# Kernel tuning notes

Measured on AMD Instinct MI355X. Metric: run time of the kernel, lower is better.

## Reference

```python
import jax, jax.numpy as jnp
import numpy as np

BN_EPS = 1e-5

def _bn(x, gamma, beta):
    # BatchNorm1d in training mode: batch mean, biased variance
    m = jnp.mean(x, axis=0)
    v = jnp.var(x, axis=0)
    return (x - m) * jax.lax.rsqrt(v + BN_EPS) * gamma + beta

def setup_inputs() -> dict:
    key = jax.random.key(0)
    ks = jax.random.split(key, 12)
    N, E, D, ED = 50000, 600000, 128, 16
    s = lambda k, sh: jax.random.normal(k, sh, dtype=jnp.float32) * 0.05
    return {
        'h': jax.random.normal(ks[0], (N, D), dtype=jnp.float32),
        'edge_index': jax.random.randint(ks[1], (2, E), 0, N, dtype=jnp.int64),
        'edge_attr': jax.random.normal(ks[2], (E, ED), dtype=jnp.float32),
        'ee_w1': s(ks[3], (ED, D)), 'ee_b1': jnp.zeros((D,), jnp.float32),
        'ee_g1': jnp.ones((D,), jnp.float32), 'ee_bb1': jnp.zeros((D,), jnp.float32),
        'ee_w2': s(ks[4], (D, D)), 'ee_b2': jnp.zeros((D,), jnp.float32),
        'mlp_w1': s(ks[5], (D, D)), 'mlp_b1': jnp.zeros((D,), jnp.float32),
        'mlp_g1': jnp.ones((D,), jnp.float32), 'mlp_bb1': jnp.zeros((D,), jnp.float32),
        'mlp_w2': s(ks[6], (D, D)), 'mlp_b2': jnp.zeros((D,), jnp.float32),
        'mlp_g2': jnp.ones((D,), jnp.float32), 'mlp_bb2': jnp.zeros((D,), jnp.float32),
    }

def reference(h, edge_index, edge_attr, ee_w1, ee_b1, ee_g1, ee_bb1, ee_w2, ee_b2,
              mlp_w1, mlp_b1, mlp_g1, mlp_bb1, mlp_w2, mlp_b2, mlp_g2, mlp_bb2):
    N = h.shape[0]
    src, dst = edge_index[0], edge_index[1]
    # edge_encoder: Linear -> BN -> ReLU -> Linear
    e = jax.nn.relu(_bn(edge_attr @ ee_w1 + ee_b1, ee_g1, ee_bb1)) @ ee_w2 + ee_b2  # [E, D]
    # scatter-add edge embeddings to destination nodes
    agg_edge = jax.ops.segment_sum(e, dst, num_segments=N)  # [N, D]
    h = h + agg_edge
    # GINConv (eps=0): mlp(h + sum_{j->i} h_j)
    neigh = jax.ops.segment_sum(h[src], dst, num_segments=N)  # [N, D]
    z = h + neigh
    z = jax.nn.relu(_bn(z @ mlp_w1 + mlp_b1, mlp_g1, mlp_bb1))
    z = jax.nn.relu(_bn(z @ mlp_w2 + mlp_b2, mlp_g2, mlp_bb2))
    return z
```

## Files before the change

kernel.cpp:

```cpp
#include <hip/hip_runtime.h>
#include <hip/hip_bf16.h>

#define DD 128
#define EDIM 16
#define WPB 4
#define PSE 68
#define ZST 136
#define NCOPY 16

typedef short v8s __attribute__((ext_vector_type(8)));
typedef float v4f __attribute__((ext_vector_type(4)));

__device__ __forceinline__ float ldf(const void* p, int i, int bf){
  return bf ? __bfloat162float(((const __hip_bfloat16*)p)[i])
            : ((const float*)p)[i];
}
__device__ __forceinline__ float bfu_lo(unsigned u){
  unsigned b = (u & 0xffffu) << 16; float f; __builtin_memcpy(&f,&b,4); return f;
}
__device__ __forceinline__ float bfu_hi(unsigned u){
  unsigned b = u & 0xffff0000u; float f; __builtin_memcpy(&f,&b,4); return f;
}
__device__ __forceinline__ unsigned short f2bf(float f){
  unsigned u; __builtin_memcpy(&u,&f,4);
  unsigned r = (u + 0x7fffu + ((u>>16)&1u)) >> 16;
  return (unsigned short)r;
}
__device__ __forceinline__ unsigned packbf(float a, float b){
  return (unsigned)f2bf(a) | ((unsigned)f2bf(b) << 16);
}

__global__ void k_detect(const void* g1, const int* ei, int E, int* flags){
  __shared__ int nz;
  if (threadIdx.x==0) nz = 0;
  __syncthreads();
  long long total = 2LL*E;
  long long stride = (total/1024) & ~1LL;
  if (stride < 2) stride = 2;
  long long idx = (long long)threadIdx.x*stride + 1;
  if (idx < total && ei[idx] != 0) atomicAdd(&nz, 1);
  __syncthreads();
  if (threadIdx.x==0){
    unsigned w = *(const unsigned*)g1;
    flags[0] = (w == 0x3F803F80u) ? 1 : 0;
    flags[1] = (nz == 0) ? 1 : 0;
  }
}

__global__ void k_transB(const void* w0, const void* w1, const void* w2,
                         const void* we1, const int* __restrict__ flags,
                         short* __restrict__ Bt){
  const int bf = flags[0];
  for (int idx = blockIdx.x*blockDim.x + threadIdx.x; idx < 3*16384 + 2048;
       idx += gridDim.x*blockDim.x){
    if (idx < 3*16384){
      int m = idx >> 14, r = idx & 16383;
      int nn = r >> 7, k = r & 127;
      const void* w = (m==0) ? w0 : ((m==1) ? w1 : w2);
      Bt[idx] = (short)f2bf(ldf(w, k*DD + nn, bf));
    } else {
      int r = idx - 3*16384;
      int nn = r >> 4, k = r & 15;
      Bt[idx] = (short)f2bf(ldf(we1, k*DD + nn, bf));
    }
  }
}

__global__ __launch_bounds__(256) void k_attr_moments(
    const void* __restrict__ attr, int E, const int* __restrict__ flags,
    float* __restrict__ Ssum , float* __restrict__ csum )
{
  __shared__ short Ws[4*512];
  __shared__ float sred[4][256];
  __shared__ float credu[4][16];
  const int t = threadIdx.x;
  const int wv = t >> 6, lane = t & 63, l15 = lane & 15, quad = lane >> 4;
  const int bf = flags[0];
  const int el = lane >> 1, half = lane & 1;
  short* W = &Ws[wv*512];

  v4f acc = (v4f){0.f,0.f,0.f,0.f};
  float cs[8];
  #pragma unroll
  for (int j=0;j<8;++j) cs[j]=0.f;

  const int nchunks = (E + 31) >> 5;
  for (int c = blockIdx.x*4 + wv; c < nchunks; c += gridDim.x*4){
    const int e = c*32 + el;
    const bool ok = (e < E);
    float f[8];
    if (bf){
      uint4 u = {0u,0u,0u,0u};
      if (ok) u = reinterpret_cast<const uint4*>(attr)[(size_t)e*2 + half];
      f[0]=bfu_lo(u.x); f[1]=bfu_hi(u.x); f[2]=bfu_lo(u.y); f[3]=bfu_hi(u.y);
      f[4]=bfu_lo(u.z); f[5]=bfu_hi(u.z); f[6]=bfu_lo(u.w); f[7]=bfu_hi(u.w);
    } else {
      float4 v0 = {0,0,0,0}, v1 = {0,0,0,0};
      if (ok){
        const float4* ap = reinterpret_cast<const float4*>(attr) +
                           (size_t)e*4 + half*2;
        v0 = ap[0]; v1 = ap[1];
      }
      f[0]=v0.x; f[1]=v0.y; f[2]=v0.z; f[3]=v0.w;
      f[4]=v1.x; f[5]=v1.y; f[6]=v1.z; f[7]=v1.w;
    }
    #pragma unroll
    for (int j=0;j<8;++j){
      cs[j] += f[j];
      W[(half*8 + j)*32 + el] = (short)f2bf(f[j]);
    }
    v8s a = *reinterpret_cast<const v8s*>(&W[l15*32 + quad*8]);
    acc = __builtin_amdgcn_mfma_f32_16x16x32_bf16(a, a, acc, 0,0,0);
  }

  #pragma unroll
  for (int r=0;r<4;++r) sred[wv][(quad*4 + r)*16 + l15] = acc[r];
  #pragma unroll
  for (int j=0;j<8;++j){
    #pragma unroll
    for (int off=2; off<64; off<<=1) cs[j] += __shfl_xor(cs[j], off, 64);
  }
  if (lane < 2){
    #pragma unroll
    for (int j=0;j<8;++j) credu[wv][lane*8 + j] = cs[j];
  }
  __syncthreads();
  const int cp = blockIdx.x & (NCOPY-1);
  float s = sred[0][t]+sred[1][t]+sred[2][t]+sred[3][t];
  atomicAdd(&Ssum[cp*256 + t], s);
  if (t < 16){
    float s2 = credu[0][t]+credu[1][t]+credu[2][t]+credu[3][t];
    atomicAdd(&csum[cp*16 + t], s2);
  }
}

__global__ void k_edge_bn(const void* __restrict__ w1, const void* __restrict__ g,
                          const void* __restrict__ bb,
                          const float* __restrict__ Ssum, const float* __restrict__ csum,
                          float Einv, const int* __restrict__ flags,
                          float* __restrict__ sc, float* __restrict__ sh){
  __shared__ float fS[256];
  __shared__ float fc[16];
  const int j = threadIdx.x;
  const int bf = flags[0];
  {
    float a0 = 0.f, a1 = 0.f;
    #pragma unroll
    for (int c=0;c<NCOPY;++c){ a0 += Ssum[c*256 + j]; a1 += Ssum[c*256 + 128 + j]; }
    fS[j] = a0; fS[128+j] = a1;
    if (j < 16){
      float a2 = 0.f;
      #pragma unroll
      for (int c=0;c<NCOPY;++c) a2 += csum[c*16 + j];
      fc[j] = a2;
    }
  }
  __syncthreads();
  float w[EDIM];
  #pragma unroll
  for (int p=0;p<EDIM;++p) w[p] = ldf(w1, p*DD + j, bf);
  float mu0 = 0.f;
  #pragma unroll
  for (int p=0;p<EDIM;++p) mu0 += fc[p]*Einv*w[p];
  float s2 = 0.f;
  #pragma unroll
  for (int p=0;p<EDIM;++p){
    float acc = 0.f;
    #pragma unroll
    for (int q=0;q<EDIM;++q) acc += fS[p*16 + q]*w[q];
    s2 += w[p]*acc;
  }
  float var = s2*Einv - mu0*mu0;
  float scv = ldf(g, j, bf) * rsqrtf(var + 1e-5f);
  sc[j] = scv;
  sh[j] = ldf(bb, j, bf) - mu0*scv;
}

__global__ void k_hist(const int* __restrict__ ei, int E,
                       const int* __restrict__ flags, int* __restrict__ deg){
  const int i64 = flags[1];
  const int2* ei2 = (const int2*)ei;
  for (int e = blockIdx.x*blockDim.x + threadIdx.x; e < E;
       e += gridDim.x*blockDim.x){
    int d = i64 ? ei2[E + e].x : ei[E + e];
    atomicAdd(&deg[d], 1);
  }
}

__global__ void k_scan_partial(const int* __restrict__ deg, int n,
                               int* __restrict__ bsum){
  __shared__ int red[256];
  const int t = threadIdx.x;
  const int base = blockIdx.x*1024;
  int s = 0;
  for (int i = t; i < 1024; i += 256){
    int g = base + i;
    s += (g < n) ? deg[g] : 0;
  }
  red[t] = s; __syncthreads();
  for (int off=128; off>0; off>>=1){
    if (t < off) red[t] += red[t+off];
    __syncthreads();
  }
  if (t==0) bsum[blockIdx.x] = red[0];
}

__global__ void k_scan_tops(int* __restrict__ bsum, int nb, int* __restrict__ total){
  __shared__ int buf[256];
  const int t = threadIdx.x;
  int v = (t < nb) ? bsum[t] : 0;
  buf[t] = v; __syncthreads();
  for (int off=1; off<256; off<<=1){
    int x = (t>=off) ? buf[t-off] : 0;
    __syncthreads();
    buf[t] += x; __syncthreads();
  }
  if (t < nb) bsum[t] = buf[t] - v;
  if (t == 255) *total = buf[255];
}

__global__ void k_scan_final(const int* __restrict__ deg, int n,
                             const int* __restrict__ bsum, const int* __restrict__ total,
                             int* __restrict__ offsets, int* __restrict__ cursor,
                             int* __restrict__ win2node){
  __shared__ int red[256];
  const int t = threadIdx.x;
  const int base = blockIdx.x*1024 + t*4;
  int v[4]; int s = 0;
  #pragma unroll
  for (int k=0;k<4;++k){
    int g = base + k;
    v[k] = (g < n) ? deg[g] : 0;
    s += v[k];
  }
  red[t] = s; __syncthreads();
  for (int off=1; off<256; off<<=1){
    int x = (t>=off) ? red[t-off] : 0;
    __syncthreads();
    red[t] += x; __syncthreads();
  }
  int ex = bsum[blockIdx.x] + red[t] - s;
  #pragma unroll
  for (int k=0;k<4;++k){
    int g = base + k;
    if (g < n){
      offsets[g] = ex; cursor[g] = ex;
      int end = ex + v[k];
      for (int w = (ex + 63) >> 6; (w << 6) < end; ++w) win2node[w] = g;
    }
    ex += v[k];
  }
  if (blockIdx.x==0 && t==0) offsets[n] = *total;
}

__global__ void k_scatter(const int* __restrict__ ei, int E,
                          const int* __restrict__ flags,
                          int* __restrict__ cursor, int2* __restrict__ se){
  const int i64 = flags[1];
  const int2* ei2 = (const int2*)ei;
  for (int e = blockIdx.x*blockDim.x + threadIdx.x; e < E;
       e += gridDim.x*blockDim.x){
    int d = i64 ? ei2[E + e].x : ei[E + e];
    int s = i64 ? ei2[e].x     : ei[e];
    int pp = atomicAdd(&cursor[d], 1);
    se[pp] = make_int2(s, e);
  }
}

__global__ __launch_bounds__(256) void k_edgeagg(
    const void* __restrict__ attr, const int2* __restrict__ se,
    const short* __restrict__ w1t,
    const float* __restrict__ sc, const float* __restrict__ sh,
    const int* __restrict__ offsets, const int* __restrict__ win2node,
    const int* __restrict__ flags, int n, int E, float* __restrict__ Pagg)
{
  __shared__ __align__(16) float Ps[DD*PSE];
  const int t = threadIdx.x;
  const int wv = t >> 6, lane = t & 63, l15 = lane & 15, quad = lane >> 4;
  const int bf = flags[0];
  const int G0 = blockIdx.x * (64*WPB);
  if (G0 >= E) return;

  v8s afrag[WPB];
  #pragma unroll
  for (int w=0; w<WPB; ++w){
    afrag[w] = (v8s){0,0,0,0,0,0,0,0};
    if (quad < 2){
      int slot = G0 + w*64 + wv*16 + l15;
      if (slot < E){
        int e = se[slot].y;
        if (bf){
          afrag[w] = *reinterpret_cast<const v8s*>(
                (const short*)attr + (size_t)e*EDIM + quad*8);
        } else {
          const float4* ap = reinterpret_cast<const float4*>(
                (const float*)attr + (size_t)e*EDIM + quad*8);
          float4 v0 = ap[0], v1 = ap[1];
          v8s av;
          av[0]=(short)f2bf(v0.x); av[1]=(short)f2bf(v0.y);
          av[2]=(short)f2bf(v0.z); av[3]=(short)f2bf(v0.w);
          av[4]=(short)f2bf(v1.x); av[5]=(short)f2bf(v1.y);
          av[6]=(short)f2bf(v1.z); av[7]=(short)f2bf(v1.w);
          afrag[w] = av;
        }
      }
    }
  }

  v8s bfrag[8];
  #pragma unroll
  for (int cg=0;cg<8;++cg){
    bfrag[cg] = (v8s){0,0,0,0,0,0,0,0};
    if (quad < 2)
      bfrag[cg] = *reinterpret_cast<const v8s*>(&w1t[(cg*16+l15)*EDIM + quad*8]);
  }
  const float scA = sc[lane],      shA = sh[lane];
  const float scB = sc[lane + 64], shB = sh[lane + 64];

  #pragma unroll
  for (int w=0; w<WPB; ++w){
    const int B0 = G0 + w*64;
    if (B0 >= E) break;
    const int Bend = (B0 + 64 < E) ? (B0 + 64) : E;

    #pragma unroll
    for (int cg=0;cg<8;++cg){
      v4f acc = (v4f){0.f,0.f,0.f,0.f};
      acc = __builtin_amdgcn_mfma_f32_16x16x32_bf16(bfrag[cg], afrag[w], acc, 0,0,0);
      #pragma unroll
      for (int reg=0;reg<4;++reg)
        Ps[(cg*16 + quad*4 + reg)*PSE + wv*16 + l15] = acc[reg];
    }
    __syncthreads();

    const int i0 = win2node[blockIdx.x*WPB + w];
    for (int idx = i0 + wv; idx < n; idx += 4){
      const int nb = offsets[idx], ne = offsets[idx+1];
      if (nb >= Bend) break;
      int s0 = nb - B0; if (s0 < 0) s0 = 0;
      const int s1 = (ne < Bend ? ne : Bend) - B0;
      if (s1 <= s0) continue;
      float sa = 0.f, sb = 0.f;
      const int c1 = (s1 - 1) >> 2;
      for (int cc = s0 >> 2; cc <= c1; ++cc){
        v4f va = *reinterpret_cast<const v4f*>(&Ps[lane*PSE + cc*4]);
        v4f vb = *reinterpret_cast<const v4f*>(&Ps[(lane+64)*PSE + cc*4]);
        #pragma unroll
        for (int k2=0;k2<4;++k2){
          const int r = cc*4 + k2;
          if (r >= s0 && r < s1){
            sa += fmaxf(fmaf(va[k2], scA, shA), 0.f);
            sb += fmaxf(fmaf(vb[k2], scB, shB), 0.f);
          }
        }
      }
      if (nb < B0 || ne > Bend){
        atomicAdd(&Pagg[(size_t)idx*DD + lane], sa);
        atomicAdd(&Pagg[(size_t)idx*DD + lane + 64], sb);
      } else {
        Pagg[(size_t)idx*DD + lane] = sa;
        Pagg[(size_t)idx*DD + lane + 64] = sb;
      }
    }
    __syncthreads();
  }
}

__global__ __launch_bounds__(256) void k_gemm_y1(
    const uint4* __restrict__ hnew16, const int* __restrict__ offsets,
    const int2* __restrict__ se, const short* __restrict__ Bt,
    const void* __restrict__ bias, const int* __restrict__ flags, int n,
    __hip_bfloat16* __restrict__ out, float* __restrict__ stats)
{
  __shared__ __align__(16) short Zs[64*ZST];
  __shared__ float sb[256];
  const int t = threadIdx.x;
  const int bfi = flags[0];
  sb[t] = 0.f;
  const int wv = t >> 6, lane = t & 63, l15 = lane & 15, quad = lane >> 4;
  const int g = lane >> 4, c16 = lane & 15;
  const int R0 = blockIdx.x*64;

  for (int k = 0; k < 16; ++k){
    const int i = R0 + wv*16 + k;
    uint4 o = {0u,0u,0u,0u};
    if (i < n){
      const int beg = offsets[i], end = offsets[i+1];
      float a0=0.f,a1=0.f,a2=0.f,a3=0.f,a4=0.f,a5=0.f,a6=0.f,a7=0.f;
      int c0 = beg;
      for (; c0 + 8 <= end; c0 += 8){
        int s1 = se[c0 + g].x;
        int s2 = se[c0 + 4 + g].x;
        uint4 u = hnew16[(size_t)s1*16 + c16];
        uint4 v = hnew16[(size_t)s2*16 + c16];
        a0 += bfu_lo(u.x)+bfu_lo(v.x); a1 += bfu_hi(u.x)+bfu_hi(v.x);
        a2 += bfu_lo(u.y)+bfu_lo(v.y); a3 += bfu_hi(u.y)+bfu_hi(v.y);
        a4 += bfu_lo(u.z)+bfu_lo(v.z); a5 += bfu_hi(u.z)+bfu_hi(v.z);
        a6 += bfu_lo(u.w)+bfu_lo(v.w); a7 += bfu_hi(u.w)+bfu_hi(v.w);
      }
      for (; c0 < end; c0 += 4){
        int r = c0 + g;
        if (r < end){
          uint4 u = hnew16[(size_t)se[r].x*16 + c16];
          a0 += bfu_lo(u.x); a1 += bfu_hi(u.x);
          a2 += bfu_lo(u.y); a3 += bfu_hi(u.y);
          a4 += bfu_lo(u.z); a5 += bfu_hi(u.z);
          a6 += bfu_lo(u.w); a7 += bfu_hi(u.w);
        }
      }
      a0 += __shfl_xor(a0,16,64); a1 += __shfl_xor(a1,16,64);
      a2 += __shfl_xor(a2,16,64); a3 += __shfl_xor(a3,16,64);
      a4 += __shfl_xor(a4,16,64); a5 += __shfl_xor(a5,16,64);
      a6 += __shfl_xor(a6,16,64); a7 += __shfl_xor(a7,16,64);
      a0 += __shfl_xor(a0,32,64); a1 += __shfl_xor(a1,32,64);
      a2 += __shfl_xor(a2,32,64); a3 += __shfl_xor(a3,32,64);
      a4 += __shfl_xor(a4,32,64); a5 += __shfl_xor(a5,32,64);
      a6 += __shfl_xor(a6,32,64); a7 += __shfl_xor(a7,32,64);
      if (lane < 16){
        uint4 m = hnew16[(size_t)i*16 + lane];
        o.x = packbf(a0+bfu_lo(m.x), a1+bfu_hi(m.x));
        o.y = packbf(a2+bfu_lo(m.y), a3+bfu_hi(m.y));
        o.z = packbf(a4+bfu_lo(m.z), a5+bfu_hi(m.z));
        o.w = packbf(a6+bfu_lo(m.w), a7+bfu_hi(m.w));
      }
    }
    if (lane < 16)
      *reinterpret_cast<uint4*>(&Zs[(wv*16 + k)*ZST + lane*8]) = o;
  }
  __syncthreads();

  v8s a[4];
  #pragma unroll
  for (int ks=0;ks<4;++ks)
    a[ks] = *reinterpret_cast<const v8s*>(
        &Zs[(wv*16 + l15)*ZST + ks*32 + quad*8]);

  v4f acc[8];
  #pragma unroll
  for (int cg=0;cg<8;++cg) acc[cg] = (v4f){0.f,0.f,0.f,0.f};
  #pragma unroll
  for (int ks=0;ks<4;++ks){
    #pragma unroll
    for (int cg=0;cg<8;++cg){
      v8s b = *reinterpret_cast<const v8s*>(
                &Bt[(cg*16+l15)*DD + ks*32 + quad*8]);
      acc[cg] = __builtin_amdgcn_mfma_f32_16x16x32_bf16(a[ks], b, acc[cg], 0,0,0);
    }
  }

  float bc[8];
  #pragma unroll
  for (int cg=0;cg<8;++cg) bc[cg] = ldf(bias, cg*16 + l15, bfi);
  float ss[8], sq[8];
  #pragma unroll
  for (int cg=0;cg<8;++cg){ ss[cg]=0.f; sq[cg]=0.f; }

  #pragma unroll
  for (int reg=0;reg<4;++reg){
    const int row = R0 + wv*16 + quad*4 + reg;
    if (row < n){
      #pragma unroll
      for (int cg=0;cg<8;++cg){
        const int col = cg*16 + l15;
        float x = acc[cg][reg] + bc[cg];
        out[(size_t)row*DD + col] = __float2bfloat16(x);
        ss[cg] += x; sq[cg] += x*x;
      }
    }
  }

  #pragma unroll
  for (int cg=0;cg<8;++cg){
    float s = ss[cg], q = sq[cg];
    s += __shfl_xor(s, 16, 64); s += __shfl_xor(s, 32, 64);
    q += __shfl_xor(q, 16, 64); q += __shfl_xor(q, 32, 64);
    if (quad == 0){
      atomicAdd(&sb[cg*16 + l15], s);
      atomicAdd(&sb[128 + cg*16 + l15], q);
    }
  }
  __syncthreads();
  atomicAdd(&stats[t], sb[t]);
}

__global__ __launch_bounds__(256) void k_gemm_mfma(
    const short* __restrict__ A, const float* __restrict__ Af32,
    const short* __restrict__ Bt, const void* __restrict__ bias,
    const float* __restrict__ psc, const float* __restrict__ psh,
    const int* __restrict__ deg, const void* __restrict__ H,
    const int* __restrict__ flags, int n,
    __hip_bfloat16* __restrict__ out, float* __restrict__ stats, int mode)
{
  __shared__ float sb[256];
  const int t = threadIdx.x;
  const int bfi = flags[0];
  sb[t] = 0.f;
  __syncthreads();
  const int wv = t >> 6, lane = t & 63, l15 = lane & 15, quad = lane >> 4;
  const int R0 = blockIdx.x*64 + wv*16;

  v8s a[4];
  {
    const int arow = R0 + l15;
    const bool ok = (arow < n);
    #pragma unroll
    for (int ks=0;ks<4;++ks){
      const int k0 = ks*32 + quad*8;
      float f[8];
      if (Af32){
        float4 v0 = {0,0,0,0}, v1 = {0,0,0,0};
        if (ok){
          const float4* ap = reinterpret_cast<const float4*>(
              Af32 + (size_t)arow*DD + k0);
          v0 = ap[0]; v1 = ap[1];
        }
        f[0]=v0.x; f[1]=v0.y; f[2]=v0.z; f[3]=v0.w;
        f[4]=v1.x; f[5]=v1.y; f[6]=v1.z; f[7]=v1.w;
        v8s av;
        #pragma unroll
        for (int j=0;j<8;++j) av[j] = (short)f2bf(f[j]);
        a[ks] = av;
      } else {
        uint4 u = {0u,0u,0u,0u};
        if (ok) u = *reinterpret_cast<const uint4*>(&A[(size_t)arow*DD + k0]);
        if (psc){
          f[0]=bfu_lo(u.x); f[1]=bfu_hi(u.x); f[2]=bfu_lo(u.y); f[3]=bfu_hi(u.y);
          f[4]=bfu_lo(u.z); f[5]=bfu_hi(u.z); f[6]=bfu_lo(u.w); f[7]=bfu_hi(u.w);
          v8s av;
          #pragma unroll
          for (int j=0;j<8;++j)
            av[j] = (short)f2bf(fmaxf(fmaf(f[j], psc[k0+j], psh[k0+j]), 0.f));
          a[ks] = av;
        } else {
          a[ks] = *reinterpret_cast<v8s*>(&u);
        }
      }
    }
  }

  v4f acc[8];
  #pragma unroll
  for (int cg=0;cg<8;++cg) acc[cg] = (v4f){0.f,0.f,0.f,0.f};
  #pragma unroll
  for (int ks=0;ks<4;++ks){
    #pragma unroll
    for (int cg=0;cg<8;++cg){
      v8s b = *reinterpret_cast<const v8s*>(
                &Bt[(cg*16+l15)*DD + ks*32 + quad*8]);
      acc[cg] = __builtin_amdgcn_mfma_f32_16x16x32_bf16(a[ks], b, acc[cg], 0,0,0);
    }
  }

  float bc[8];
  #pragma unroll
  for (int cg=0;cg<8;++cg) bc[cg] = ldf(bias, cg*16 + l15, bfi);
  float ss[8], sq[8];
  #pragma unroll
  for (int cg=0;cg<8;++cg){ ss[cg]=0.f; sq[cg]=0.f; }

  #pragma unroll
  for (int reg=0;reg<4;++reg){
    const int row = R0 + quad*4 + reg;
    if (row < n){
      float degf = (mode==1) ? (float)deg[row] : 0.f;
      #pragma unroll
      for (int cg=0;cg<8;++cg){
        const int col = cg*16 + l15;
        float x = acc[cg][reg];
        if (mode==1) x = fmaf(degf, bc[cg], x) + ldf(H, (size_t)row*DD + col, bfi);
        else         x += bc[cg];
        out[(size_t)row*DD + col] = __float2bfloat16(x);
        ss[cg] += x; sq[cg] += x*x;
      }
    }
  }

  if (stats){
    #pragma unroll
    for (int cg=0;cg<8;++cg){
      float s = ss[cg], q = sq[cg];
      s += __shfl_xor(s, 16, 64); s += __shfl_xor(s, 32, 64);
      q += __shfl_xor(q, 16, 64); q += __shfl_xor(q, 32, 64);
      if (quad == 0){
        atomicAdd(&sb[cg*16 + l15], s);
        atomicAdd(&sb[128 + cg*16 + l15], q);
      }
    }
    __syncthreads();
    atomicAdd(&stats[t], sb[t]);
  }
}

__global__ void k_bn_params(const float* __restrict__ stats, const void* __restrict__ g,
                            const void* __restrict__ bb, const int* __restrict__ flags,
                            float inv_n, float* __restrict__ sc, float* __restrict__ sh){
  const int j = threadIdx.x;
  const int bf = flags[0];
  float mean = stats[j]*inv_n;
  float var  = stats[DD+j]*inv_n - mean*mean;
  float s = ldf(g, j, bf) * rsqrtf(var + 1e-5f);
  sc[j] = s;
  sh[j] = ldf(bb, j, bf) - mean*s;
}

__global__ void k_final(const unsigned* __restrict__ yH,
                        const float* __restrict__ sc, const float* __restrict__ sh,
                        int n, const int* __restrict__ flags, void* __restrict__ out){
  const int bf = flags[0];
  const int nw = n*64;
  for (int i = blockIdx.x*blockDim.x + threadIdx.x; i < nw;
       i += gridDim.x*blockDim.x){
    const int j0 = (i & 63)*2;
    unsigned u = yH[i];
    float v0 = fmaxf(fmaf(bfu_lo(u), sc[j0],   sh[j0]),   0.f);
    float v1 = fmaxf(fmaf(bfu_hi(u), sc[j0+1], sh[j0+1]), 0.f);
    if (bf){
      ((unsigned*)out)[i] = packbf(v0, v1);
    } else {
      *reinterpret_cast<float2*>((float*)out + 2*(size_t)i) = make_float2(v0, v1);
    }
  }
}

extern "C" void kernel_launch(void* const* d_in, const int* in_sizes, int n_in,
                              void* d_out, int out_size, void* d_ws, size_t ws_size,
                              hipStream_t stream)
{
  const void* h       = d_in[0];
  const int*  ei      = (const int*)d_in[1];
  const void* attr    = d_in[2];
  const void* ee_w1   = d_in[3];
  const void* ee_g1   = d_in[5];
  const void* ee_bb1  = d_in[6];
  const void* ee_w2   = d_in[7];
  const void* ee_b2   = d_in[8];
  const void* mlp_w1  = d_in[9];
  const void* mlp_b1  = d_in[10];
  const void* mlp_g1  = d_in[11];
  const void* mlp_bb1 = d_in[12];
  const void* mlp_w2  = d_in[13];
  const void* mlp_b2  = d_in[14];
  const void* mlp_g2  = d_in[15];
  const void* mlp_bb2 = d_in[16];

  const int N = in_sizes[0] / DD;
  const int E = in_sizes[1] / 2;
  const int nb = (N + 1023) / 1024;
  const int e64  = (E + 63) / 64;
  const int e256 = (E + 64*WPB - 1) / (64*WPB);

  char* p = (char*)d_ws;
  auto alloc = [&](size_t bytes)->char*{
    char* r = p;
    p += (bytes + 255) & ~size_t(255);
    return r;
  };
  int* flags = (int*)alloc(8);
  char* zbase = p;
  int*   deg    = (int*)  zbase;
  float* csum   = (float*)(zbase + (size_t)N*4);
  float* Ssum   = (float*)(zbase + (size_t)N*4 + 1024);
  float* stats1 = (float*)(zbase + (size_t)N*4 + 1024 + 16384);
  float* stats2 = (float*)(zbase + (size_t)N*4 + 1024 + 16384 + 1024);
  float* Pagg   = (float*)(zbase + (size_t)N*4 + 1024 + 16384 + 2048);
  size_t zlen   = (size_t)N*4 + 1024 + 16384 + 2048 + (size_t)N*DD*4;
  p += (zlen + 255) & ~size_t(255);
  int*   bsum     = (int*)  alloc(256*4);
  int*   total    = (int*)  alloc(64);
  int*   offsets  = (int*)  alloc((size_t)(N+1)*4);
  int*   cursor   = (int*)  alloc((size_t)N*4);
  int*   win2node = (int*)  alloc((size_t)(e64 + 8)*4);
  int2*  se       = (int2*) alloc((size_t)E*8);
  short* Bt      = (short*)alloc((size_t)(3*DD*DD + DD*EDIM)*2);
  short* w1t     = Bt + 3*DD*DD;
  float* ebn_sc  = (float*)alloc(512);
  float* ebn_sh  = (float*)alloc(512);
  float* sc1     = (float*)alloc(512);
  float* sh1     = (float*)alloc(512);
  float* sc2     = (float*)alloc(512);
  float* sh2     = (float*)alloc(512);
  short* hnewH   = (short*)alloc((size_t)N*DD*2);
  short* y1H     = (short*)alloc((size_t)N*DD*2);
  short* y2H     = (short*)alloc((size_t)N*DD*2);
  (void)ws_size; (void)n_in; (void)out_size;

  const int g64  = (N + 63) / 64;

  hipMemsetAsync(zbase, 0, zlen, stream);
  k_detect<<<1, 1024, 0, stream>>>(ee_g1, ei, E, flags);
  k_transB<<<208, 256, 0, stream>>>(ee_w2, mlp_w1, mlp_w2, ee_w1, flags, Bt);
  k_attr_moments<<<1024, 256, 0, stream>>>(attr, E, flags, Ssum, csum);
  k_edge_bn<<<1, 128, 0, stream>>>(ee_w1, ee_g1, ee_bb1, Ssum, csum,
                                   1.0f/(float)E, flags, ebn_sc, ebn_sh);
  k_hist<<<1024, 256, 0, stream>>>(ei, E, flags, deg);
  k_scan_partial<<<nb, 256, 0, stream>>>(deg, N, bsum);
  k_scan_tops<<<1, 256, 0, stream>>>(bsum, nb, total);
  k_scan_final<<<nb, 256, 0, stream>>>(deg, N, bsum, total, offsets, cursor,
                                       win2node);
  k_scatter<<<1024, 256, 0, stream>>>(ei, E, flags, cursor, se);

  k_edgeagg<<<e256, 256, 0, stream>>>(attr, se, w1t, ebn_sc, ebn_sh,
                                      offsets, win2node, flags, N, E, Pagg);

  k_gemm_mfma<<<g64, 256, 0, stream>>>(nullptr, Pagg, Bt, ee_b2,
                                       nullptr, nullptr, deg, h, flags, N,
                                       (__hip_bfloat16*)hnewH, nullptr, 1);
  k_gemm_y1<<<g64, 256, 0, stream>>>((const uint4*)hnewH, offsets, se,
                                     Bt + 16384, mlp_b1, flags, N,
                                     (__hip_bfloat16*)y1H, stats1);
  k_bn_params<<<1, 128, 0, stream>>>(stats1, mlp_g1, mlp_bb1, flags,
                                     1.0f/(float)N, sc1, sh1);
  k_gemm_mfma<<<g64, 256, 0, stream>>>(y1H, nullptr, Bt + 32768, mlp_b2,
                                       sc1, sh1, nullptr, nullptr,
                                       flags, N, (__hip_bfloat16*)y2H, stats2, 0);
  k_bn_params<<<1, 128, 0, stream>>>(stats2, mlp_g2, mlp_bb2, flags,
                                     1.0f/(float)N, sc2, sh2);

  k_final<<<2048, 256, 0, stream>>>((const unsigned*)y2H, sc2, sh2,
                                    N, flags, d_out);
}
```

Measured before the change: 454.9 us.

## Gather neighbor sums via flat edge-parallel LDS atomics instead of per-row wave loops

Replaces the per-destination-row gather loop (each wave processes 16 rows serially with shuffles) with a block-wide edge-parallel scheme. The 64-row tile's edge sources and a local row map are staged into shared memory, then 16 thread groups each gather one source row and accumulate into an fp32 LDS tile with shared-memory atomics, with a binary-search fallback when the block has more than CAP edges. This balances work across uneven degrees and exposes more independent loads. In exchange it adds LDS atomic contention, a larger fp32 shared tile that may reduce occupancy, and an extra fp32-to-bf16 conversion before the MFMA.

```diff
diff --git a/kernel.cpp b/kernel.cpp
--- a/kernel.cpp
+++ b/kernel.cpp
@@ -5,7 +5,8 @@
 #define EDIM 16
 #define WPB 4
 #define PSE 68
-#define ZST 136
+#define ZAS 132
+#define CAP 1536
 #define NCOPY 16
 
 typedef short v8s __attribute__((ext_vector_type(8)));
@@ -372,68 +373,97 @@
     const void* __restrict__ bias, const int* __restrict__ flags, int n,
     __hip_bfloat16* __restrict__ out, float* __restrict__ stats)
 {
-  __shared__ __align__(16) short Zs[64*ZST];
+  __shared__ __align__(16) float Zacc[64*ZAS];
+  __shared__ int sesrc[CAP];
+  __shared__ unsigned char smap[CAP];
+  __shared__ int offc[65];
   __shared__ float sb[256];
   const int t = threadIdx.x;
   const int bfi = flags[0];
   sb[t] = 0.f;
   const int wv = t >> 6, lane = t & 63, l15 = lane & 15, quad = lane >> 4;
-  const int g = lane >> 4, c16 = lane & 15;
   const int R0 = blockIdx.x*64;
 
-  for (int k = 0; k < 16; ++k){
-    const int i = R0 + wv*16 + k;
-    uint4 o = {0u,0u,0u,0u};
-    if (i < n){
-      const int beg = offsets[i], end = offsets[i+1];
-      float a0=0.f,a1=0.f,a2=0.f,a3=0.f,a4=0.f,a5=0.f,a6=0.f,a7=0.f;
-      int c0 = beg;
-      for (; c0 + 8 <= end; c0 += 8){
-        int s1 = se[c0 + g].x;
-        int s2 = se[c0 + 4 + g].x;
-        uint4 u = hnew16[(size_t)s1*16 + c16];
-        uint4 v = hnew16[(size_t)s2*16 + c16];
-        a0 += bfu_lo(u.x)+bfu_lo(v.x); a1 += bfu_hi(u.x)+bfu_hi(v.x);
-        a2 += bfu_lo(u.y)+bfu_lo(v.y); a3 += bfu_hi(u.y)+bfu_hi(v.y);
-        a4 += bfu_lo(u.z)+bfu_lo(v.z); a5 += bfu_hi(u.z)+bfu_hi(v.z);
-        a6 += bfu_lo(u.w)+bfu_lo(v.w); a7 += bfu_hi(u.w)+bfu_hi(v.w);
-      }
-      for (; c0 < end; c0 += 4){
-        int r = c0 + g;
-        if (r < end){
-          uint4 u = hnew16[(size_t)se[r].x*16 + c16];
-          a0 += bfu_lo(u.x); a1 += bfu_hi(u.x);
-          a2 += bfu_lo(u.y); a3 += bfu_hi(u.y);
-          a4 += bfu_lo(u.z); a5 += bfu_hi(u.z);
-          a6 += bfu_lo(u.w); a7 += bfu_hi(u.w);
-        }
-      }
-      a0 += __shfl_xor(a0,16,64); a1 += __shfl_xor(a1,16,64);
-      a2 += __shfl_xor(a2,16,64); a3 += __shfl_xor(a3,16,64);
-      a4 += __shfl_xor(a4,16,64); a5 += __shfl_xor(a5,16,64);
-      a6 += __shfl_xor(a6,16,64); a7 += __shfl_xor(a7,16,64);
-      a0 += __shfl_xor(a0,32,64); a1 += __shfl_xor(a1,32,64);
-      a2 += __shfl_xor(a2,32,64); a3 += __shfl_xor(a3,32,64);
-      a4 += __shfl_xor(a4,32,64); a5 += __shfl_xor(a5,32,64);
-      a6 += __shfl_xor(a6,32,64); a7 += __shfl_xor(a7,32,64);
-      if (lane < 16){
-        uint4 m = hnew16[(size_t)i*16 + lane];
-        o.x = packbf(a0+bfu_lo(m.x), a1+bfu_hi(m.x));
-        o.y = packbf(a2+bfu_lo(m.y), a3+bfu_hi(m.y));
-        o.z = packbf(a4+bfu_lo(m.z), a5+bfu_hi(m.z));
-        o.w = packbf(a6+bfu_lo(m.w), a7+bfu_hi(m.w));
-      }
-    }
-    if (lane < 16)
-      *reinterpret_cast<uint4*>(&Zs[(wv*16 + k)*ZST + lane*8]) = o;
+  if (t < 65){
+    const int g = R0 + t;
+    offc[t] = offsets[(g < n) ? g : n];
+  }
+  #pragma unroll
+  for (int m=0;m<4;++m){
+    const int idx = t*4 + m;
+    const int r = idx >> 4, q = idx & 15;
+    uint4 u = {0u,0u,0u,0u};
+    if (R0 + r < n) u = hnew16[(size_t)(R0+r)*16 + q];
+    v4f p0, p1;
+    p0[0]=bfu_lo(u.x); p0[1]=bfu_hi(u.x); p0[2]=bfu_lo(u.y); p0[3]=bfu_hi(u.y);
+    p1[0]=bfu_lo(u.z); p1[1]=bfu_hi(u.z); p1[2]=bfu_lo(u.w); p1[3]=bfu_hi(u.w);
+    *reinterpret_cast<v4f*>(&Zacc[r*ZAS + q*8])     = p0;
+    *reinterpret_cast<v4f*>(&Zacc[r*ZAS + q*8 + 4]) = p1;
+  }
+  __syncthreads();
+
+  const int bs = offc[0], be = offc[64];
+  const int cnt = be - bs;
+  const int ccap = cnt < CAP ? cnt : CAP;
+  if (t < 64){
+    const int e0 = offc[t] - bs;
+    int e1 = offc[t+1] - bs; if (e1 > CAP) e1 = CAP;
+    for (int s = e0; s < e1; ++s) smap[s] = (unsigned char)t;
+  }
+  for (int s = t; s < ccap; s += 256) sesrc[s] = se[bs + s].x;
+  __syncthreads();
+
+  const int grp = t >> 4, c16 = t & 15;
+  for (int s = grp; s < ccap; s += 16){
+    const int src = sesrc[s];
+    const int dl  = smap[s];
+    const uint4 u = hnew16[(size_t)src*16 + c16];
+    float* zr = &Zacc[dl*ZAS + c16*8];
+    atomicAdd(&zr[0], bfu_lo(u.x));
+    atomicAdd(&zr[1], bfu_hi(u.x));
+    atomicAdd(&zr[2], bfu_lo(u.y));
+    atomicAdd(&zr[3], bfu_hi(u.y));
+    atomicAdd(&zr[4], bfu_lo(u.z));
+    atomicAdd(&zr[5], bfu_hi(u.z));
+    atomicAdd(&zr[6], bfu_lo(u.w));
+    atomicAdd(&zr[7], bfu_hi(u.w));
+  }
+  if (cnt > CAP){
+    for (int s = CAP + grp; s < cnt; s += 16){
+      const int gs = bs + s;
+      const int src = se[gs].x;
+      int lo = 0, hi = 63;
+      while (lo < hi){
+        const int mid = (lo + hi + 1) >> 1;
+        if (offc[mid] <= gs) lo = mid; else hi = mid - 1;
+      }
+      const uint4 u = hnew16[(size_t)src*16 + c16];
+      float* zr = &Zacc[lo*ZAS + c16*8];
+      atomicAdd(&zr[0], bfu_lo(u.x));
+      atomicAdd(&zr[1], bfu_hi(u.x));
+      atomicAdd(&zr[2], bfu_lo(u.y));
+      atomicAdd(&zr[3], bfu_hi(u.y));
+      atomicAdd(&zr[4], bfu_lo(u.z));
+      atomicAdd(&zr[5], bfu_hi(u.z));
+      atomicAdd(&zr[6], bfu_lo(u.w));
+      atomicAdd(&zr[7], bfu_hi(u.w));
+    }
   }
   __syncthreads();
 
   v8s a[4];
   #pragma unroll
-  for (int ks=0;ks<4;++ks)
-    a[ks] = *reinterpret_cast<const v8s*>(
-        &Zs[(wv*16 + l15)*ZST + ks*32 + quad*8]);
+  for (int ks=0;ks<4;++ks){
+    const float* zr = &Zacc[(wv*16 + l15)*ZAS + ks*32 + quad*8];
+    v4f p0 = *reinterpret_cast<const v4f*>(zr);
+    v4f p1 = *reinterpret_cast<const v4f*>(zr + 4);
+    v8s av;
+    av[0]=(short)f2bf(p0[0]); av[1]=(short)f2bf(p0[1]);
+    av[2]=(short)f2bf(p0[2]); av[3]=(short)f2bf(p0[3]);
+    av[4]=(short)f2bf(p1[0]); av[5]=(short)f2bf(p1[1]);
+    av[6]=(short)f2bf(p1[2]); av[7]=(short)f2bf(p1[3]);
+    a[ks] = av;
+  }
 
   v4f acc[8];
   #pragma unroll
```

Result: slower. 904.4 us (+98.8%).
